# Optimization experiments

Measured on AMD Instinct MI355X. Metric: run time of the kernel, lower is better.

## Reference

```python
import jax, jax.numpy as jnp
import numpy as np

B, S, D = 2, 1024, 1024
E, K, I = 8, 2, 1024
LIMIT = 7.0
ALPHA = 1.702


def setup_inputs() -> dict:
    key = jax.random.key(0)
    k0, k1, k2, k3 = jax.random.split(key, 4)
    return {
        "x": jax.random.normal(k0, (B, S, D), jnp.float32),
        "norm_w": jnp.ones((D,), jnp.float32),
        "gate_w": jax.random.normal(k1, (E, D), jnp.float32) / np.sqrt(D).astype(np.float32),
        "gate_b": jnp.zeros((E,), jnp.float32),
        "mlp1_w": jax.random.normal(k2, (E, 2 * I, D), jnp.float32) / np.sqrt(D).astype(np.float32),
        "mlp1_b": jnp.zeros((E, 2 * I), jnp.float32),
        "mlp2_w": jax.random.normal(k3, (E, D, I), jnp.float32) / np.sqrt(I).astype(np.float32),
        "mlp2_b": jnp.zeros((E, D), jnp.float32),
    }


def _swiglu(t, limit):
    # interleaved gate/linear split (gpt-oss style) with clamping
    glu = jnp.minimum(t[..., ::2], limit)
    lin = jnp.clip(t[..., 1::2], -limit, limit)
    return glu * jax.nn.sigmoid(ALPHA * glu) * (lin + 1.0)


def reference(x, norm_w, gate_w, gate_b, mlp1_w, mlp1_b, mlp2_w, mlp2_b):
    eps = jnp.finfo(x.dtype).eps
    # RMSNorm
    h = x * jax.lax.rsqrt(jnp.mean(x * x, axis=-1, keepdims=True) + eps) * norm_w
    flat = h.reshape(-1, D)                              # [T, D]
    # top-k gating
    logits = flat @ gate_w.T + gate_b                    # [T, E]
    vals, idx = jax.lax.top_k(logits, K)                 # sorted descending
    wts = jax.nn.softmax(vals, axis=-1)                  # [T, K]
    # per-expert SwiGLU MLP (dense over experts, identical math to per-token gather)
    t1 = jnp.einsum('td,efd->tef', flat, mlp1_w) + mlp1_b   # [T, E, 2I]
    act = _swiglu(t1, LIMIT)                                 # [T, E, I]
    y = jnp.einsum('tei,edi->ted', act, mlp2_w) + mlp2_b     # [T, E, D]
    # gather selected experts and combine
    sel = jnp.take_along_axis(y, idx[:, :, None], axis=1)    # [T, K, D]
    out = jnp.sum(sel * wts[:, :, None], axis=1).reshape(x.shape)
    return x + out
```

## Files before the change

kernel.cpp:

```cpp
#include <hip/hip_runtime.h>
#include <stdint.h>

#define TNUM 2048
#define DDIM 1024
#define NEXP 8
#define KSEL 2
#define IDIM 1024
#define TWOI 2048
#define LIMITV 7.0f
#define ALPHAV 1.702f
#define ROWT_MAX 40
#define RMSB (TNUM / 4)
#define N81 (NEXP * TWOI * DDIM / 8)
#define N82 (NEXP * DDIM * IDIM / 8)
#define G1TOT (ROWT_MAX * (TWOI / 128))
#define G2TOT (2 * ROWT_MAX * (DDIM / 128))

typedef __attribute__((ext_vector_type(8))) short bf16x8;
typedef __attribute__((ext_vector_type(4))) float f32x4;

#define VMCNT0() asm volatile("s_waitcnt vmcnt(0)" ::: "memory")
#define BARRIER() asm volatile("s_barrier" ::: "memory")

__device__ __forceinline__ unsigned short f2bf(float f) {
  unsigned u = __float_as_uint(f);
  u += 0x7FFF + ((u >> 16) & 1);
  return (unsigned short)(u >> 16);
}

__device__ __forceinline__ int4 cvt8(float4 a, float4 b) {
  union { unsigned short us[8]; int4 v; } o;
  o.us[0] = f2bf(a.x); o.us[1] = f2bf(a.y); o.us[2] = f2bf(a.z); o.us[3] = f2bf(a.w);
  o.us[4] = f2bf(b.x); o.us[5] = f2bf(b.y); o.us[6] = f2bf(b.z); o.us[7] = f2bf(b.w);
  return o.v;
}

__device__ __forceinline__ float4 ld4bf(const unsigned short* p) {
  int2 v = *(const int2*)p;
  unsigned a = (unsigned)v.x, b = (unsigned)v.y;
  float4 r;
  r.x = __uint_as_float((a & 0xFFFFu) << 16);
  r.y = __uint_as_float(a & 0xFFFF0000u);
  r.z = __uint_as_float((b & 0xFFFFu) << 16);
  r.w = __uint_as_float(b & 0xFFFF0000u);
  return r;
}

__device__ __forceinline__ void gl2lds16(const void* g, void* l) {
  __builtin_amdgcn_global_load_lds(
      (__attribute__((address_space(1))) unsigned int*)(uintptr_t)g,
      (__attribute__((address_space(3))) unsigned int*)(uintptr_t)l, 16, 0, 0);
}

__device__ __forceinline__ int xcd_swz(int bid, int total) {
  int q = total >> 3, r = total & 7;
  int xcd = bid & 7, pos = bid >> 3;
  return (xcd < r ? xcd * (q + 1) : r * (q + 1) + (xcd - r) * q) + pos;
}

__global__ __launch_bounds__(256) void k_rms_cvt(
    const float* __restrict__ x, const float* __restrict__ norm_w,
    const float* __restrict__ gate_w, const float* __restrict__ gate_b,
    const float* __restrict__ w1f, unsigned short* __restrict__ w1b,
    unsigned short* __restrict__ hb, int* __restrict__ tidx,
    float* __restrict__ twt) {
  if ((int)blockIdx.x >= RMSB) {
    int k0 = ((int)blockIdx.x - RMSB) * 1024 + (int)threadIdx.x;
    const float4* s = (const float4*)w1f;
#pragma unroll
    for (int i = 0; i < 4; ++i) {
      int k = k0 + i * 256;
      if (k < N81) ((int4*)w1b)[k] = cvt8(s[2 * k], s[2 * k + 1]);
    }
    return;
  }
  const int lane = threadIdx.x & 63;
  const int t = blockIdx.x * 4 + (threadIdx.x >> 6);

  const float4* xr  = (const float4*)x + (size_t)t * 256 + lane * 4;
  const float4* nwr = (const float4*)norm_w + lane * 4;
  const float4* gbr = (const float4*)gate_b;
  float4 xv[4], nwv[4];
#pragma unroll
  for (int i = 0; i < 4; ++i) xv[i] = xr[i];
  float4 gb0 = gbr[0], gb1 = gbr[1];
#pragma unroll
  for (int i = 0; i < 4; ++i) nwv[i] = nwr[i];

  float ss = 0.f;
#pragma unroll
  for (int i = 0; i < 4; ++i)
    ss += xv[i].x * xv[i].x + xv[i].y * xv[i].y + xv[i].z * xv[i].z + xv[i].w * xv[i].w;
#pragma unroll
  for (int m = 1; m < 64; m <<= 1) ss += __shfl_xor(ss, m);
  const float sc = rsqrtf(ss * (1.0f / DDIM) + 1.1920929e-07f);

  float4 h[4];
#pragma unroll
  for (int i = 0; i < 4; ++i) {
    h[i].x = xv[i].x * sc * nwv[i].x;
    h[i].y = xv[i].y * sc * nwv[i].y;
    h[i].z = xv[i].z * sc * nwv[i].z;
    h[i].w = xv[i].w * sc * nwv[i].w;
  }
  int4* hw = (int4*)(hb + (size_t)t * DDIM + lane * 16);
  hw[0] = cvt8(h[0], h[1]);
  hw[1] = cvt8(h[2], h[3]);

  float p[NEXP];
#pragma unroll
  for (int e = 0; e < NEXP; ++e) {
    const float4* g4 = (const float4*)gate_w + e * 256 + lane * 4;
    float4 a = g4[0], b = g4[1], c = g4[2], d = g4[3];
    p[e] = h[0].x * a.x + h[0].y * a.y + h[0].z * a.z + h[0].w * a.w
         + h[1].x * b.x + h[1].y * b.y + h[1].z * b.z + h[1].w * b.w
         + h[2].x * c.x + h[2].y * c.y + h[2].z * c.z + h[2].w * c.w
         + h[3].x * d.x + h[3].y * d.y + h[3].z * d.z + h[3].w * d.w;
  }
#pragma unroll
  for (int m = 1; m < 64; m <<= 1) {
#pragma unroll
    for (int e = 0; e < NEXP; ++e) p[e] += __shfl_xor(p[e], m);
  }
  p[0] += gb0.x; p[1] += gb0.y; p[2] += gb0.z; p[3] += gb0.w;
  p[4] += gb1.x; p[5] += gb1.y; p[6] += gb1.z; p[7] += gb1.w;

  if (lane == 0) {
    int i0 = 0; float v0 = p[0];
#pragma unroll
    for (int e = 1; e < NEXP; ++e) if (p[e] > v0) { v0 = p[e]; i0 = e; }
    int i1 = -1; float v1 = -3.4e38f;
#pragma unroll
    for (int e = 0; e < NEXP; ++e) if (e != i0 && p[e] > v1) { v1 = p[e]; i1 = e; }
    float e1 = __expf(v1 - v0);
    float w0 = 1.f / (1.f + e1);
    int2 ip; ip.x = i0; ip.y = i1;
    float2 wp; wp.x = w0; wp.y = e1 * w0;
    ((int2*)tidx)[t] = ip;
    ((float2*)twt)[t] = wp;
  }
}

__global__ __launch_bounds__(512) void k_sched(
    const int* __restrict__ tidx, int* __restrict__ meta,
    int* __restrict__ tl, int* __restrict__ rows, int* __restrict__ sof) {
  __shared__ unsigned short cnt[256][NEXP];
  __shared__ int off[NEXP];
  __shared__ int tot[NEXP];
  const int tid = threadIdx.x;
  int e_[16], rel_[16];
  if (tid < 256) {
#pragma unroll
    for (int k = 0; k < 16; ++k) e_[k] = tidx[tid * 16 + k];
#pragma unroll
    for (int k = 0; k < 16; ++k) {
      int r = 0;
#pragma unroll
      for (int j2 = 0; j2 < 16; ++j2)
        if (j2 < k) r += (e_[j2] == e_[k]) ? 1 : 0;
      rel_[k] = r;
    }
#pragma unroll
    for (int e = 0; e < NEXP; ++e) {
      int c = 0;
#pragma unroll
      for (int k = 0; k < 16; ++k) c += (e_[k] == e) ? 1 : 0;
      cnt[tid][e] = (unsigned short)c;
    }
  }
  __syncthreads();
  {
    const int we = tid >> 6, lane = tid & 63;
    int carry = 0;
#pragma unroll
    for (int chunk = 0; chunk < 4; ++chunk) {
      int i = chunk * 64 + lane;
      int c = (int)cnt[i][we];
      int s = c;
#pragma unroll
      for (int o = 1; o < 64; o <<= 1) {
        int t2 = __shfl_up(s, o);
        if (lane >= o) s += t2;
      }
      cnt[i][we] = (unsigned short)(s - c + carry);
      carry += __shfl(s, 63);
    }
    if (lane == 0) tot[we] = carry;
  }
  __syncthreads();
  if (tid == 0) {
    int acc = 0, nt = 0;
    for (int e = 0; e < NEXP; ++e) {
      meta[8 + e] = acc; off[e] = acc;
      int c = tot[e]; acc += c;
      int ntile = (c + 127) >> 7;
      for (int r = 0; r < ntile; ++r) tl[nt++] = (e << 8) | r;
    }
    meta[16] = acc;
    meta[25] = nt;
  }
  __syncthreads();
  if (tid < 256) {
#pragma unroll
    for (int k = 0; k < 16; ++k) {
      int i = tid * 16 + k;
      int e = e_[k];
      int slot = off[e] + (int)cnt[tid][e] + rel_[k];
      rows[slot] = i >> 1;
      sof[i] = slot;
    }
  }
}

__global__ __launch_bounds__(256, 2) void k_gemm1(
    const unsigned short* __restrict__ hb, const unsigned short* __restrict__ w1b,
    const float* __restrict__ mlp1_b, const int* __restrict__ meta,
    const int* __restrict__ tl, const int* __restrict__ rows,
    const float* __restrict__ w2f, unsigned short* __restrict__ w2b,
    unsigned short* __restrict__ actb) {
  const int bid = blockIdx.x;
  const int tid = threadIdx.x, lane = tid & 63, wid = tid >> 6;
  if (bid >= G1TOT) {
    int k0 = (bid - G1TOT) * 1024 + tid;
    const float4* s = (const float4*)w2f;
#pragma unroll
    for (int i = 0; i < 4; ++i) {
      int k = k0 + i * 256;
      if (k < N82) ((int4*)w2b)[k] = cvt8(s[2 * k], s[2 * k + 1]);
    }
    return;
  }
  const int nt = meta[25];
  const int total = nt * (TWOI / 128);
  if (bid >= total) return;
  const int j = xcd_swz(bid, total);
  const int ct = j / nt;
  const int tile = tl[j - ct * nt];
  const int e = tile >> 8, rt = tile & 255;
  const int offs = meta[8 + e];
  const int n_e = meta[9 + e] - offs;

  __shared__ unsigned short As[2][128][64];
  __shared__ unsigned short Bs[2][128][64];
  __shared__ int srow[128];
  if (tid < 128) srow[tid] = rows[offs + min(rt * 128 + tid, n_e - 1)];
  __syncthreads();

  const int rloc = tid >> 3;
  const int csw  = (((tid & 7) ^ (rloc & 7)) << 3);
  const unsigned short* gA[4];
  const unsigned short* gB[4];
  const unsigned short* w1e = w1b + (size_t)e * TWOI * DDIM;
#pragma unroll
  for (int jj = 0; jj < 4; ++jj) {
    gA[jj] = hb + (size_t)srow[jj * 32 + rloc] * DDIM + csw;
    gB[jj] = w1e + (size_t)(ct * 128 + jj * 32 + rloc) * DDIM + csw;
  }

#define G1_STAGE(BUF, KT)                                                      \
  _Pragma("unroll") for (int jj = 0; jj < 4; ++jj) {                           \
    gl2lds16(gA[jj] + (KT) * 64, &As[BUF][0][0] + jj * 2048 + tid * 8);        \
    gl2lds16(gB[jj] + (KT) * 64, &Bs[BUF][0][0] + jj * 2048 + tid * 8);        \
  }

  f32x4 acc[4][4];
#pragma unroll
  for (int m = 0; m < 4; ++m)
#pragma unroll
    for (int n = 0; n < 4; ++n) acc[m][n] = (f32x4){0.f, 0.f, 0.f, 0.f};

  const int wr = wid >> 1, wc = wid & 1;
  const int lrow = lane & 15, ksub = (lane >> 4) * 8;
  const int NK = DDIM / 64;

  G1_STAGE(0, 0)
  VMCNT0();
  BARRIER();
#pragma unroll
  for (int kt = 0; kt < NK; ++kt) {
    const int cur = kt & 1;
    if (kt + 1 < NK) { G1_STAGE(cur ^ 1, kt + 1) }
#pragma unroll
    for (int kk = 0; kk < 2; ++kk) {
      bf16x8 af[4], bfr[4];
#pragma unroll
      for (int m = 0; m < 4; ++m) {
        int row = wr * 64 + m * 16 + lrow;
        int chunk = ((kk * 32 + ksub) >> 3) ^ (row & 7);
        af[m] = *(const bf16x8*)&As[cur][row][chunk * 8];
      }
#pragma unroll
      for (int n = 0; n < 4; ++n) {
        int row = wc * 64 + n * 16 + lrow;
        int chunk = ((kk * 32 + ksub) >> 3) ^ (row & 7);
        bfr[n] = *(const bf16x8*)&Bs[cur][row][chunk * 8];
      }
#pragma unroll
      for (int m = 0; m < 4; ++m)
#pragma unroll
        for (int n = 0; n < 4; ++n)
          acc[m][n] = __builtin_amdgcn_mfma_f32_16x16x32_bf16(af[m], bfr[n], acc[m][n], 0, 0, 0);
    }
    if (kt + 1 < NK) { VMCNT0(); }
    BARRIER();
  }
#undef G1_STAGE

  const float* b1e = mlp1_b + e * TWOI;
#pragma unroll
  for (int m = 0; m < 4; ++m) {
#pragma unroll
    for (int n = 0; n < 4; ++n) {
      int cg = ct * 128 + wc * 64 + n * 16 + (lane & 15);
      float bias = b1e[cg];
#pragma unroll
      for (int j2 = 0; j2 < 4; ++j2) {
        float val = acc[m][n][j2] + bias;
        float part = __shfl_xor(val, 1);
        int rl = wr * 64 + m * 16 + ((lane >> 4) << 2) + j2;
        if (!(lane & 1)) {
          float glu = fminf(val, LIMITV);
          float lin = fminf(fmaxf(part, -LIMITV), LIMITV);
          float s = 1.f / (1.f + __expf(-ALPHAV * glu));
          float a = glu * s * (lin + 1.f);
          if (rt * 128 + rl < n_e)
            actb[(size_t)(offs + rt * 128 + rl) * IDIM + (cg >> 1)] = f2bf(a);
        }
      }
    }
  }
}

__global__ __launch_bounds__(256, 4) void k_gemm2(
    const unsigned short* __restrict__ actb, const unsigned short* __restrict__ w2b,
    const float* __restrict__ mlp2_b, const int* __restrict__ meta,
    const int* __restrict__ tl, unsigned short* __restrict__ ybuf) {
  const int nt = meta[25];
  const int totalK = nt * (DDIM / 128) * 2;
  const int bid = blockIdx.x;
  if (bid >= totalK) return;
  const int j = xcd_swz(bid, totalK);
  const int kp = j & 1;
  const int jt = j >> 1;
  const int ct = jt / nt;
  const int tile = tl[jt - ct * nt];
  const int e = tile >> 8, rt = tile & 255;
  const int offs = meta[8 + e];
  const int n_e = meta[9 + e] - offs;
  const int tid = threadIdx.x, lane = tid & 63, wid = tid >> 6;

  __shared__ unsigned short As[128][64];
  __shared__ unsigned short Bs[128][64];

  const int rloc = tid >> 3;
  const int csw  = (((tid & 7) ^ (rloc & 7)) << 3);
  const int koff = kp * 512;
  const unsigned short* gA[4];
  const unsigned short* gB[4];
  const unsigned short* w2e = w2b + (size_t)e * DDIM * IDIM;
#pragma unroll
  for (int jj = 0; jj < 4; ++jj) {
    gA[jj] = actb + (size_t)(offs + min(rt * 128 + jj * 32 + rloc, n_e - 1)) * IDIM + koff + csw;
    gB[jj] = w2e + (size_t)(ct * 128 + jj * 32 + rloc) * IDIM + koff + csw;
  }

#define G2_STAGE(KT)                                                           \
  _Pragma("unroll") for (int jj = 0; jj < 4; ++jj) {                           \
    gl2lds16(gA[jj] + (KT) * 64, &As[0][0] + jj * 2048 + tid * 8);             \
    gl2lds16(gB[jj] + (KT) * 64, &Bs[0][0] + jj * 2048 + tid * 8);             \
  }

  f32x4 acc[4][4];
#pragma unroll
  for (int m = 0; m < 4; ++m)
#pragma unroll
    for (int n = 0; n < 4; ++n) acc[m][n] = (f32x4){0.f, 0.f, 0.f, 0.f};

  const int wr = wid >> 1, wc = wid & 1;
  const int lrow = lane & 15, ksub = (lane >> 4) * 8;
  const int NK = 512 / 64;

#pragma unroll
  for (int kt = 0; kt < NK; ++kt) {
    G2_STAGE(kt)
    VMCNT0();
    BARRIER();
#pragma unroll
    for (int kk = 0; kk < 2; ++kk) {
      bf16x8 af[4], bfr[4];
#pragma unroll
      for (int m = 0; m < 4; ++m) {
        int row = wr * 64 + m * 16 + lrow;
        int chunk = ((kk * 32 + ksub) >> 3) ^ (row & 7);
        af[m] = *(const bf16x8*)&As[row][chunk * 8];
      }
#pragma unroll
      for (int n = 0; n < 4; ++n) {
        int row = wc * 64 + n * 16 + lrow;
        int chunk = ((kk * 32 + ksub) >> 3) ^ (row & 7);
        bfr[n] = *(const bf16x8*)&Bs[row][chunk * 8];
      }
#pragma unroll
      for (int m = 0; m < 4; ++m)
#pragma unroll
        for (int n = 0; n < 4; ++n)
          acc[m][n] = __builtin_amdgcn_mfma_f32_16x16x32_bf16(af[m], bfr[n], acc[m][n], 0, 0, 0);
    }
    BARRIER();
  }
#undef G2_STAGE

  const float* b2e = mlp2_b + e * DDIM;
  unsigned short* yh = ybuf + (size_t)kp * TNUM * KSEL * DDIM;
#pragma unroll
  for (int m = 0; m < 4; ++m) {
#pragma unroll
    for (int n = 0; n < 4; ++n) {
      int d = ct * 128 + wc * 64 + n * 16 + (lane & 15);
      float bias = kp ? 0.f : b2e[d];
#pragma unroll
      for (int j2 = 0; j2 < 4; ++j2) {
        int rl = wr * 64 + m * 16 + ((lane >> 4) << 2) + j2;
        if (rt * 128 + rl < n_e)
          yh[(size_t)(offs + rt * 128 + rl) * DDIM + d] = f2bf(acc[m][n][j2] + bias);
      }
    }
  }
}

__global__ __launch_bounds__(256) void k_combine(
    const float* __restrict__ x, const unsigned short* __restrict__ ybuf,
    const int* __restrict__ sof, const float* __restrict__ twt,
    float* __restrict__ out) {
  int t = blockIdx.x, tid = threadIdx.x;
  int s0 = sof[2 * t], s1 = sof[2 * t + 1];
  float w0 = twt[2 * t], w1 = twt[2 * t + 1];
  const size_t H = (size_t)TNUM * KSEL * DDIM;
  float4 xv = ((const float4*)x)[t * 256 + tid];
  float4 a0 = ld4bf(ybuf + (size_t)s0 * DDIM + tid * 4);
  float4 a1 = ld4bf(ybuf + H + (size_t)s0 * DDIM + tid * 4);
  float4 b0 = ld4bf(ybuf + (size_t)s1 * DDIM + tid * 4);
  float4 b1 = ld4bf(ybuf + H + (size_t)s1 * DDIM + tid * 4);
  float4 o;
  o.x = xv.x + w0 * (a0.x + a1.x) + w1 * (b0.x + b1.x);
  o.y = xv.y + w0 * (a0.y + a1.y) + w1 * (b0.y + b1.y);
  o.z = xv.z + w0 * (a0.z + a1.z) + w1 * (b0.z + b1.z);
  o.w = xv.w + w0 * (a0.w + a1.w) + w1 * (b0.w + b1.w);
  ((float4*)out)[t * 256 + tid] = o;
}

extern "C" void kernel_launch(void* const* d_in, const int* in_sizes, int n_in,
                              void* d_out, int out_size, void* d_ws, size_t ws_size,
                              hipStream_t stream) {
  const float* x      = (const float*)d_in[0];
  const float* norm_w = (const float*)d_in[1];
  const float* gate_w = (const float*)d_in[2];
  const float* gate_b = (const float*)d_in[3];
  const float* mlp1_w = (const float*)d_in[4];
  const float* mlp1_b = (const float*)d_in[5];
  const float* mlp2_w = (const float*)d_in[6];
  const float* mlp2_b = (const float*)d_in[7];
  float* out = (float*)d_out;

  char* w = (char*)d_ws;
  unsigned short* w1b = (unsigned short*)w; w += (size_t)NEXP * TWOI * DDIM * 2;
  unsigned short* w2b = (unsigned short*)w; w += (size_t)NEXP * DDIM * IDIM * 2;
  unsigned short* hb  = (unsigned short*)w; w += (size_t)TNUM * DDIM * 2;
  unsigned short* actb = (unsigned short*)w; w += (size_t)TNUM * KSEL * IDIM * 2;
  unsigned short* ybuf = (unsigned short*)w; w += (size_t)2 * TNUM * KSEL * DDIM * 2;
  int*   tidx = (int*)w;  w += TNUM * KSEL * 4;
  float* twt  = (float*)w; w += TNUM * KSEL * 4;
  int*   sof  = (int*)w;  w += TNUM * KSEL * 4;
  int*   rows = (int*)w;  w += TNUM * KSEL * 4;
  int*   meta = (int*)w;  w += 32 * 4;
  int*   tl   = (int*)w;  w += 64 * 4;

  k_rms_cvt<<<RMSB + N81 / 1024, 256, 0, stream>>>(x, norm_w, gate_w, gate_b,
                                                   mlp1_w, w1b, hb, tidx, twt);
  k_sched<<<1, 512, 0, stream>>>(tidx, meta, tl, rows, sof);
  k_gemm1<<<G1TOT + N82 / 1024, 256, 0, stream>>>(hb, w1b, mlp1_b, meta, tl, rows,
                                                  mlp2_w, w2b, actb);
  k_gemm2<<<G2TOT, 256, 0, stream>>>(actb, w2b, mlp2_b, meta, tl, ybuf);
  k_combine<<<TNUM, 256, 0, stream>>>(x, ybuf, sof, twt, out);
}
```

Before: 109.3 us.

## Halve gemm1 K-tile, raise occupancy, and overlap prefetch with partial vmcnt waits

The expert up-projection GEMM now works on 32-wide K tiles instead of 64, halving its LDS footprint. The launch bound is raised from 2 to 4 blocks per CU to allow more resident waves. The full vmcnt(0) wait after issuing the next stage is replaced by vmcnt(4), so only the current stage's loads must land, and sched barriers keep the compiler from moving code across the sync points. The trade-offs are twice as many loop iterations with two workgroup barriers each, a narrower XOR swizzle that may bring back LDS bank conflicts, and tighter register limits that could cause spills.

```diff
diff --git a/kernel.cpp b/kernel.cpp
--- a/kernel.cpp
+++ b/kernel.cpp
@@ -19,8 +19,11 @@
 typedef __attribute__((ext_vector_type(8))) short bf16x8;
 typedef __attribute__((ext_vector_type(4))) float f32x4;
 
+#define VMCNT4() asm volatile("s_waitcnt vmcnt(4)" ::: "memory")
 #define VMCNT0() asm volatile("s_waitcnt vmcnt(0)" ::: "memory")
 #define BARRIER() asm volatile("s_barrier" ::: "memory")
+#define WGBAR() __builtin_amdgcn_s_barrier()
+#define SCHEDB() __builtin_amdgcn_sched_barrier(0)
 
 __device__ __forceinline__ unsigned short f2bf(float f) {
   unsigned u = __float_as_uint(f);
@@ -212,7 +215,7 @@
   }
 }
 
-__global__ __launch_bounds__(256, 2) void k_gemm1(
+__global__ __launch_bounds__(256, 4) void k_gemm1(
     const unsigned short* __restrict__ hb, const unsigned short* __restrict__ w1b,
     const float* __restrict__ mlp1_b, const int* __restrict__ meta,
     const int* __restrict__ tl, const int* __restrict__ rows,
@@ -240,27 +243,25 @@
   const int offs = meta[8 + e];
   const int n_e = meta[9 + e] - offs;
 
-  __shared__ unsigned short As[2][128][64];
-  __shared__ unsigned short Bs[2][128][64];
+  __shared__ unsigned short As[2][128][32];
+  __shared__ unsigned short Bs[2][128][32];
   __shared__ int srow[128];
   if (tid < 128) srow[tid] = rows[offs + min(rt * 128 + tid, n_e - 1)];
   __syncthreads();
 
-  const int rloc = tid >> 3;
-  const int csw  = (((tid & 7) ^ (rloc & 7)) << 3);
-  const unsigned short* gA[4];
-  const unsigned short* gB[4];
+  const int r0  = tid >> 2;
+  const int csw = (((tid & 3) ^ (r0 & 3)) << 3);
   const unsigned short* w1e = w1b + (size_t)e * TWOI * DDIM;
-#pragma unroll
-  for (int jj = 0; jj < 4; ++jj) {
-    gA[jj] = hb + (size_t)srow[jj * 32 + rloc] * DDIM + csw;
-    gB[jj] = w1e + (size_t)(ct * 128 + jj * 32 + rloc) * DDIM + csw;
-  }
-
-#define G1_STAGE(BUF, KT)                                                      \
-  _Pragma("unroll") for (int jj = 0; jj < 4; ++jj) {                           \
-    gl2lds16(gA[jj] + (KT) * 64, &As[BUF][0][0] + jj * 2048 + tid * 8);        \
-    gl2lds16(gB[jj] + (KT) * 64, &Bs[BUF][0][0] + jj * 2048 + tid * 8);        \
+  const unsigned short* gA0 = hb + (size_t)srow[r0] * DDIM + csw;
+  const unsigned short* gA1 = hb + (size_t)srow[64 + r0] * DDIM + csw;
+  const unsigned short* gB0 = w1e + (size_t)(ct * 128 + r0) * DDIM + csw;
+  const unsigned short* gB1 = w1e + (size_t)(ct * 128 + 64 + r0) * DDIM + csw;
+
+#define G1_STAGE(BUF, KT) {                                                    \
+    gl2lds16(gA0 + (KT) * 32, &As[BUF][0][0] + tid * 8);                       \
+    gl2lds16(gA1 + (KT) * 32, &As[BUF][0][0] + 2048 + tid * 8);                \
+    gl2lds16(gB0 + (KT) * 32, &Bs[BUF][0][0] + tid * 8);                       \
+    gl2lds16(gB1 + (KT) * 32, &Bs[BUF][0][0] + 2048 + tid * 8);                \
   }
 
   f32x4 acc[4][4];
@@ -270,39 +271,44 @@
     for (int n = 0; n < 4; ++n) acc[m][n] = (f32x4){0.f, 0.f, 0.f, 0.f};
 
   const int wr = wid >> 1, wc = wid & 1;
-  const int lrow = lane & 15, ksub = (lane >> 4) * 8;
-  const int NK = DDIM / 64;
+  const int lrow = lane & 15, kgrp = lane >> 4;
+  const int NK = DDIM / 32;
 
   G1_STAGE(0, 0)
-  VMCNT0();
-  BARRIER();
 #pragma unroll
   for (int kt = 0; kt < NK; ++kt) {
     const int cur = kt & 1;
-    if (kt + 1 < NK) { G1_STAGE(cur ^ 1, kt + 1) }
-#pragma unroll
-    for (int kk = 0; kk < 2; ++kk) {
-      bf16x8 af[4], bfr[4];
-#pragma unroll
-      for (int m = 0; m < 4; ++m) {
-        int row = wr * 64 + m * 16 + lrow;
-        int chunk = ((kk * 32 + ksub) >> 3) ^ (row & 7);
-        af[m] = *(const bf16x8*)&As[cur][row][chunk * 8];
-      }
-#pragma unroll
-      for (int n = 0; n < 4; ++n) {
-        int row = wc * 64 + n * 16 + lrow;
-        int chunk = ((kk * 32 + ksub) >> 3) ^ (row & 7);
-        bfr[n] = *(const bf16x8*)&Bs[cur][row][chunk * 8];
-      }
-#pragma unroll
-      for (int m = 0; m < 4; ++m)
-#pragma unroll
-        for (int n = 0; n < 4; ++n)
-          acc[m][n] = __builtin_amdgcn_mfma_f32_16x16x32_bf16(af[m], bfr[n], acc[m][n], 0, 0, 0);
-    }
-    if (kt + 1 < NK) { VMCNT0(); }
-    BARRIER();
+    if (kt + 1 < NK) {
+      G1_STAGE(cur ^ 1, kt + 1)
+      SCHEDB();
+      VMCNT4();
+    } else {
+      VMCNT0();
+    }
+    SCHEDB();
+    WGBAR();
+    SCHEDB();
+    bf16x8 af[4], bfr[4];
+#pragma unroll
+    for (int m = 0; m < 4; ++m) {
+      int row = wr * 64 + m * 16 + lrow;
+      int chunk = kgrp ^ (row & 3);
+      af[m] = *(const bf16x8*)&As[cur][row][chunk * 8];
+    }
+#pragma unroll
+    for (int n = 0; n < 4; ++n) {
+      int row = wc * 64 + n * 16 + lrow;
+      int chunk = kgrp ^ (row & 3);
+      bfr[n] = *(const bf16x8*)&Bs[cur][row][chunk * 8];
+    }
+#pragma unroll
+    for (int m = 0; m < 4; ++m)
+#pragma unroll
+      for (int n = 0; n < 4; ++n)
+        acc[m][n] = __builtin_amdgcn_mfma_f32_16x16x32_bf16(af[m], bfr[n], acc[m][n], 0, 0, 0);
+    SCHEDB();
+    WGBAR();
+    SCHEDB();
   }
 #undef G1_STAGE
 
```

New measurement: 105.3 us. 1.04x faster.
